# Kernel tuning notes

Hardware: AMD Instinct MI355X
Metric: run time of the kernel (lower is better)

Reference implementation:

```python
import jax, jax.numpy as jnp
import numpy as np

N_NODES = 50000
N_EDGES = 1600000
N_PAIRS = 4096
IN_N, IN_E = 32, 8
H, OE, ON = 4, 8, 32  # heads, out_edge_feats, out_node_feats
L = 4  # layers


def setup_inputs() -> dict:
    key = jax.random.key(0)
    ks = jax.random.split(key, 20)
    s = 0.1
    return {
        "x": jax.random.normal(ks[0], (N_NODES, IN_N), jnp.float32),
        "e": jax.random.normal(ks[1], (N_EDGES, IN_E), jnp.float32),
        "W_ni": jax.random.normal(ks[2], (L, IN_N, H * OE), jnp.float32) * s,
        "W_nj": jax.random.normal(ks[3], (L, IN_N, H * OE), jnp.float32) * s,
        "W_fij": jax.random.normal(ks[4], (L, IN_E, H * OE), jnp.float32) * s,
        "b_edge": jax.random.normal(ks[5], (L, H * OE), jnp.float32) * s,
        "attn": jax.random.normal(ks[6], (L, H, OE), jnp.float32) * s,
        "W_node": jax.random.normal(ks[7], (L, IN_N, H * ON), jnp.float32) * s,
        "W1": jax.random.normal(ks[8], (2 * L * ON, 128), jnp.float32) * s,
        "b1": jax.random.normal(ks[9], (128,), jnp.float32) * s,
        "W2": jax.random.normal(ks[10], (128, 1), jnp.float32) * s,
        "b2": jax.random.normal(ks[11], (1,), jnp.float32) * s,
        "src": jax.random.randint(ks[12], (N_EDGES,), 0, N_NODES, jnp.int32),
        "dst": jax.random.randint(ks[13], (N_EDGES,), 0, N_NODES, jnp.int32),
        "users": jax.random.randint(ks[14], (N_PAIRS,), 0, N_NODES, jnp.int32),
        "items": jax.random.randint(ks[15], (N_PAIRS,), 0, N_NODES, jnp.int32),
    }


def _egat_layer(h, e, src, dst, W_ni, W_nj, W_fij, b_edge, attn, W_node, n_nodes):
    # per-edge edge features: f_ni[src] + f_nj[dst] + f_fij + bias  -> (E, H*OE)
    f = (h @ W_ni)[src] + (h @ W_nj)[dst] + e @ W_fij + b_edge
    f_out = jax.nn.leaky_relu(f).reshape(-1, H, OE)          # (E, H, OE)
    logits = jnp.einsum("ehd,hd->eh", f_out, attn)           # (E, H)
    # edge softmax over incoming edges of each dst node
    mx = jax.ops.segment_max(logits, dst, num_segments=n_nodes)
    z = jnp.exp(logits - mx[dst])
    denom = jax.ops.segment_sum(z, dst, num_segments=n_nodes)
    a = z / denom[dst]                                        # (E, H)
    hh = (h @ W_node).reshape(n_nodes, H, ON)                 # (N, H, ON)
    msg = hh[src] * a[:, :, None]                             # (E, H, ON)
    return jax.ops.segment_sum(msg, dst, num_segments=n_nodes)  # (N, H, ON)


def reference(x, e, W_ni, W_nj, W_fij, b_edge, attn, W_node, W1, b1, W2, b2,
              src, dst, users, items):
    n_nodes = x.shape[0]
    states = []
    h = x
    for l in range(L):
        agg = _egat_layer(h, e, src, dst, W_ni[l], W_nj[l], W_fij[l],
                          b_edge[l], attn[l], W_node[l], n_nodes)
        h = jax.nn.elu(agg.sum(axis=1))  # sum heads, ELU -> (N, ON)
        states.append(h)
    states = jnp.concatenate(states, axis=1)                  # (N, L*ON)
    z = jnp.concatenate([states[users], states[items]], axis=1)  # (B, 2*L*ON)
    z = jax.nn.relu(z @ W1 + b1)
    out = jax.nn.sigmoid(z @ W2 + b2)
    return out[:, 0]
```

## Files before the change

kernel.cpp:

```cpp
#include <hip/hip_runtime.h>
#include <math.h>


static __device__ inline unsigned short f2bf(float f) {
  unsigned x = __float_as_uint(f);
  unsigned r = x + 0x7fffu + ((x >> 16) & 1u);
  return (unsigned short)(r >> 16);
}
static __device__ inline float bf2f(unsigned short u) {
  return __uint_as_float(((unsigned)u) << 16);
}
static __device__ inline float bf_lo(unsigned u) {
  return __uint_as_float(u << 16);
}
static __device__ inline float bf_hi(unsigned u) {
  return __uint_as_float(u & 0xffff0000u);
}


__global__ void zero_ints(int* __restrict__ p, int n) {
  int i = blockIdx.x * blockDim.x + threadIdx.x;
  if (i < n) p[i] = 0;
}

__global__ void histogram(const int* __restrict__ dst, int* __restrict__ hist,
                          int n_edges) {
  int e = blockIdx.x * blockDim.x + threadIdx.x;
  if (e < n_edges) atomicAdd(&hist[dst[e]], 1);
}

__global__ void scan_block(const int* __restrict__ hist, int* __restrict__ partial,
                           int* __restrict__ blocksum, int n) {
  __shared__ int buf[1024];
  int tid = threadIdx.x;
  int g = blockIdx.x * 1024 + tid;
  int v = (g < n) ? hist[g] : 0;
  buf[tid] = v;
  __syncthreads();
  for (int off = 1; off < 1024; off <<= 1) {
    int t = (tid >= off) ? buf[tid - off] : 0;
    __syncthreads();
    buf[tid] += t;
    __syncthreads();
  }
  if (g < n) partial[g] = buf[tid] - v;
  if (tid == 1023) blocksum[blockIdx.x] = buf[1023];
}

__global__ void scan_sums(int* __restrict__ blocksum, int nb) {
  if (threadIdx.x == 0 && blockIdx.x == 0) {
    int run = 0;
    for (int i = 0; i < nb; i++) {
      int t = blocksum[i];
      blocksum[i] = run;
      run += t;
    }
    blocksum[nb] = run;
  }
}

__global__ void scan_add(int* __restrict__ partial ,
                         const int* __restrict__ blocksum,
                         int* __restrict__ cursor, int n, int nb) {
  int g = blockIdx.x * blockDim.x + threadIdx.x;
  if (g < n) {
    int val = partial[g] + blocksum[g >> 10];
    partial[g] = val;
    cursor[g] = val;
  }
  if (g == 0) partial[n] = blocksum[nb];
}

__global__ void fill_records(const int* __restrict__ src, const int* __restrict__ dst,
                             int* __restrict__ cursor, int2* __restrict__ rec,
                             int n_edges) {
  int e = blockIdx.x * blockDim.x + threadIdx.x;
  if (e >= n_edges) return;
  int d = dst[e];
  int p = atomicAdd(&cursor[d], 1);
  rec[p] = make_int2(src[e], e);
}


__global__ void node_proj(const float* __restrict__ h,
                          const float* __restrict__ Wni,
                          const float* __restrict__ Wnj,
                          const float* __restrict__ Wnode,
                          unsigned short* __restrict__ fni,
                          unsigned short* __restrict__ fnj,
                          unsigned short* __restrict__ hh, int n_nodes) {
  int wave = (blockIdx.x * blockDim.x + threadIdx.x) >> 6;
  int lane = threadIdx.x & 63;
  int nwaves = (gridDim.x * blockDim.x) >> 6;
  int j = lane & 31;
  const float* Wsel = (lane < 32) ? Wni : Wnj;
  for (int n = wave; n < n_nodes; n += nwaves) {
    const float* hrow = h + (size_t)n * 32;
    float a0 = 0.f, a1 = 0.f, a2 = 0.f;
#pragma unroll
    for (int k = 0; k < 32; k++) {
      float hv = hrow[k];
      a0 += hv * Wsel[k * 32 + j];
      a1 += hv * Wnode[k * 128 + lane];
      a2 += hv * Wnode[k * 128 + lane + 64];
    }
    if (lane < 32) fni[(size_t)n * 32 + j] = f2bf(a0);
    else           fnj[(size_t)n * 32 + j] = f2bf(a0);
    hh[(size_t)n * 128 + lane] = f2bf(a1);
    hh[(size_t)n * 128 + lane + 64] = f2bf(a2);
  }
}

__global__ void node_agg_fused(const int2* __restrict__ rec,
                               const int* __restrict__ row_off,
                               const unsigned short* __restrict__ fni,
                               const unsigned short* __restrict__ fnj,
                               const unsigned short* __restrict__ hh,
                               const float* __restrict__ e,
                               const float* __restrict__ Wf,
                               const float* __restrict__ bE,
                               const float* __restrict__ attn,
                               float* __restrict__ hcur,
                               float* __restrict__ states,
                               int l, int n_nodes) {
  int n = (blockIdx.x * blockDim.x + threadIdx.x) >> 6;
  int lane = threadIdx.x & 63;
  if (n >= n_nodes) return;
  int j = lane & 31;
  int head = lane >> 4;
  int lane2 = lane * 2;

  float wcol[8];
#pragma unroll
  for (int kk = 0; kk < 8; kk++) wcol[kk] = Wf[kk * 32 + j];
  float bEj = bE[j];
  float attnj = attn[j];
  float fnjv = bf2f(fnj[(size_t)n * 32 + j]);

  int base = row_off[n], end = row_off[n + 1];
  float accx = 0.f, accy = 0.f, dh = 0.f;

  for (int k2 = base; k2 < end; k2 += 2) {
    int myk = k2 + (lane >> 5);
    bool valid = myk < end;
    int ksafe = valid ? myk : base;
    int2 re = rec[ksafe];
    int s = re.x;
    const float4* ep = (const float4*)(e + (size_t)re.y * 8);
    float4 ev0 = ep[0], ev1 = ep[1];
    float fniv = bf2f(fni[(size_t)s * 32 + j]);
    float f = fniv + fnjv + bEj;
    f = fmaf(ev0.x, wcol[0], f); f = fmaf(ev0.y, wcol[1], f);
    f = fmaf(ev0.z, wcol[2], f); f = fmaf(ev0.w, wcol[3], f);
    f = fmaf(ev1.x, wcol[4], f); f = fmaf(ev1.y, wcol[5], f);
    f = fmaf(ev1.z, wcol[6], f); f = fmaf(ev1.w, wcol[7], f);
    f = (f >= 0.f) ? f : 0.01f * f;
    float lgp = f * attnj;
    lgp += __shfl_xor(lgp, 1);
    lgp += __shfl_xor(lgp, 2);
    lgp += __shfl_xor(lgp, 4);
    float z = valid ? __expf(lgp) : 0.f;
    int sA = __shfl(s, 0);
    int sB = __shfl(s, 32);
    float zA = __shfl(z, head * 8);
    float zB = __shfl(z, 32 + head * 8);
    unsigned hA = *(const unsigned*)(hh + (size_t)sA * 128 + lane2);
    accx = fmaf(bf_lo(hA), zA, accx);
    accy = fmaf(bf_hi(hA), zA, accy);
    dh += zA;
    unsigned hB = *(const unsigned*)(hh + (size_t)sB * 128 + lane2);
    accx = fmaf(bf_lo(hB), zB, accx);
    accy = fmaf(bf_hi(hB), zB, accy);
    dh += zB;
  }

  float vx = 0.f, vy = 0.f;
  if (dh > 0.f) { vx = accx / dh; vy = accy / dh; }
  vx += __shfl_xor(vx, 16); vx += __shfl_xor(vx, 32);
  vy += __shfl_xor(vy, 16); vy += __shfl_xor(vy, 32);
  if (lane < 16) {
    float rx = (vx > 0.f) ? vx : expm1f(vx);
    float ry = (vy > 0.f) ? vy : expm1f(vy);
    float2 r = make_float2(rx, ry);
    ((float2*)(hcur + (size_t)n * 32))[lane] = r;
    ((float2*)(states + (size_t)n * 128 + l * 32))[lane] = r;
  }
}

__global__ void mlp_head(const float* __restrict__ states,
                         const int* __restrict__ users, const int* __restrict__ items,
                         const float* __restrict__ W1, const float* __restrict__ b1,
                         const float* __restrict__ W2, const float* __restrict__ b2,
                         float* __restrict__ out, int n_pairs) {
  __shared__ float zin[256];
  __shared__ float red[2];
  int p = blockIdx.x;
  if (p >= n_pairs) return;
  int t = threadIdx.x;
  int u = users[p], it = items[p];
  zin[t] = states[(size_t)u * 128 + t];
  zin[t + 128] = states[(size_t)it * 128 + t];
  __syncthreads();
  float acc = b1[t];
#pragma unroll 8
  for (int i = 0; i < 256; i++) acc += zin[i] * W1[i * 128 + t];
  acc = acc > 0.f ? acc : 0.f;
  float c = acc * W2[t];
#pragma unroll
  for (int off = 32; off > 0; off >>= 1) c += __shfl_down(c, off);
  if ((t & 63) == 0) red[t >> 6] = c;
  __syncthreads();
  if (t == 0) {
    float sum = red[0] + red[1] + b2[0];
    out[p] = 1.f / (1.f + expf(-sum));
  }
}


extern "C" void kernel_launch(void* const* d_in, const int* in_sizes, int n_in,
                              void* d_out, int out_size, void* d_ws, size_t ws_size,
                              hipStream_t stream) {
  const float* x     = (const float*)d_in[0];
  const float* e     = (const float*)d_in[1];
  const float* W_ni  = (const float*)d_in[2];
  const float* W_nj  = (const float*)d_in[3];
  const float* W_fij = (const float*)d_in[4];
  const float* b_e   = (const float*)d_in[5];
  const float* attn  = (const float*)d_in[6];
  const float* W_nd  = (const float*)d_in[7];
  const float* W1    = (const float*)d_in[8];
  const float* b1    = (const float*)d_in[9];
  const float* W2    = (const float*)d_in[10];
  const float* b2    = (const float*)d_in[11];
  const int* src   = (const int*)d_in[12];
  const int* dst   = (const int*)d_in[13];
  const int* users = (const int*)d_in[14];
  const int* items = (const int*)d_in[15];
  float* out = (float*)d_out;

  int n_nodes = in_sizes[0] / 32;
  int n_edges = in_sizes[12];
  int n_pairs = in_sizes[14];

  char* wsb = (char*)d_ws;
  size_t off = 0;
  auto alloc = [&](size_t bytes) {
    char* p = wsb + off;
    off = (off + bytes + 255) & ~(size_t)255;
    return p;
  };
  float*          hcur   = (float*)alloc((size_t)n_nodes * 32 * 4);
  float*          states = (float*)alloc((size_t)n_nodes * 128 * 4);
  unsigned short* fni    = (unsigned short*)alloc((size_t)n_nodes * 32 * 2);
  unsigned short* fnj    = (unsigned short*)alloc((size_t)n_nodes * 32 * 2);
  unsigned short* hh     = (unsigned short*)alloc((size_t)n_nodes * 128 * 2);
  int2*           rec    = (int2*)alloc((size_t)n_edges * 8);
  int*            row_off  = (int*)alloc(((size_t)n_nodes + 8) * 4);
  int*            cursor   = (int*)alloc(((size_t)n_nodes + 8) * 4);
  int*            hist     = (int*)alloc(((size_t)n_nodes + 8) * 4);
  int*            blocksum = (int*)alloc(256 * 4);

  int nb = (n_nodes + 1023) / 1024;
  zero_ints<<<(n_nodes + 255) / 256, 256, 0, stream>>>(hist, n_nodes);
  histogram<<<(n_edges + 255) / 256, 256, 0, stream>>>(dst, hist, n_edges);
  scan_block<<<nb, 1024, 0, stream>>>(hist, row_off, blocksum, n_nodes);
  scan_sums<<<1, 64, 0, stream>>>(blocksum, nb);
  scan_add<<<(n_nodes + 255) / 256, 256, 0, stream>>>(row_off, blocksum, cursor,
                                                      n_nodes, nb);
  fill_records<<<(n_edges + 255) / 256, 256, 0, stream>>>(src, dst, cursor, rec,
                                                          n_edges);

  for (int l = 0; l < 4; l++) {
    const float* hin = (l == 0) ? x : hcur;
    node_proj<<<2048, 256, 0, stream>>>(hin, W_ni + l * 1024, W_nj + l * 1024,
                                        W_nd + l * 4096, fni, fnj, hh, n_nodes);
    node_agg_fused<<<(n_nodes * 64 + 255) / 256, 256, 0, stream>>>(
        rec, row_off, fni, fnj, hh, e, W_fij + l * 256, b_e + l * 32,
        attn + l * 32, hcur, states, l, n_nodes);
  }
  mlp_head<<<n_pairs, 128, 0, stream>>>(states, users, items, W1, b1, W2, b2,
                                        out, n_pairs);
}
```

Before: 961.8 us.

## Split edge attention into per-edge kernel with pre-sorted bf16 edge data

Edges are permuted once into dst-sorted order, with src, dst and bf16-packed edge features stored contiguously, so later layers read them without going through an indirection. A new per-edge kernel computes the four head attention exponentials with one thread per edge, using weights staged in shared memory. The aggregation kernel then only gathers the precomputed z values and the hh rows, staging chunks in LDS and making the source index wave-uniform. The edge bias is folded into the dst projection. The trade-off is an extra kernel launch and a 16-byte-per-edge z buffer written and read every layer, and storing edge features in bf16 lowers precision.

Result: no change. 964.5 us (+0.3%).

```diff
diff --git a/kernel.cpp b/kernel.cpp
--- a/kernel.cpp
+++ b/kernel.cpp
@@ -7,8 +7,8 @@
   unsigned r = x + 0x7fffu + ((x >> 16) & 1u);
   return (unsigned short)(r >> 16);
 }
-static __device__ inline float bf2f(unsigned short u) {
-  return __uint_as_float(((unsigned)u) << 16);
+static __device__ inline unsigned pack2bf(float lo, float hi) {
+  return (unsigned)f2bf(lo) | ((unsigned)f2bf(hi) << 16);
 }
 static __device__ inline float bf_lo(unsigned u) {
   return __uint_as_float(u << 16);
@@ -71,14 +71,31 @@
   if (g == 0) partial[n] = blocksum[nb];
 }
 
-__global__ void fill_records(const int* __restrict__ src, const int* __restrict__ dst,
-                             int* __restrict__ cursor, int2* __restrict__ rec,
-                             int n_edges) {
+__global__ void fill_perm(const int* __restrict__ dst, int* __restrict__ cursor,
+                          int* __restrict__ perm, int n_edges) {
   int e = blockIdx.x * blockDim.x + threadIdx.x;
   if (e >= n_edges) return;
-  int d = dst[e];
-  int p = atomicAdd(&cursor[d], 1);
-  rec[p] = make_int2(src[e], e);
+  int p = atomicAdd(&cursor[dst[e]], 1);
+  perm[p] = e;
+}
+
+__global__ void expand_sorted(const int* __restrict__ perm,
+                              const int* __restrict__ src,
+                              const int* __restrict__ dst,
+                              const float* __restrict__ e,
+                              int* __restrict__ src_s, int* __restrict__ dst_s,
+                              uint4* __restrict__ e_s, int n_edges) {
+  int k = blockIdx.x * blockDim.x + threadIdx.x;
+  if (k >= n_edges) return;
+  int eid = perm[k];
+  src_s[k] = src[eid];
+  dst_s[k] = dst[eid];
+  const float4* ep = (const float4*)(e + (size_t)eid * 8);
+  float4 a = ep[0], b = ep[1];
+  uint4 r;
+  r.x = pack2bf(a.x, a.y); r.y = pack2bf(a.z, a.w);
+  r.z = pack2bf(b.x, b.y); r.w = pack2bf(b.z, b.w);
+  e_s[k] = r;
 }
 
 
@@ -86,8 +103,9 @@
                           const float* __restrict__ Wni,
                           const float* __restrict__ Wnj,
                           const float* __restrict__ Wnode,
+                          const float* __restrict__ bE,
                           unsigned short* __restrict__ fni,
-                          unsigned short* __restrict__ fnj,
+                          unsigned short* __restrict__ cdst,
                           unsigned short* __restrict__ hh, int n_nodes) {
   int wave = (blockIdx.x * blockDim.x + threadIdx.x) >> 6;
   int lane = threadIdx.x & 63;
@@ -105,73 +123,120 @@
       a2 += hv * Wnode[k * 128 + lane + 64];
     }
     if (lane < 32) fni[(size_t)n * 32 + j] = f2bf(a0);
-    else           fnj[(size_t)n * 32 + j] = f2bf(a0);
+    else           cdst[(size_t)n * 32 + j] = f2bf(a0 + bE[j]);
     hh[(size_t)n * 128 + lane] = f2bf(a1);
     hh[(size_t)n * 128 + lane + 64] = f2bf(a2);
   }
 }
 
-__global__ void node_agg_fused(const int2* __restrict__ rec,
-                               const int* __restrict__ row_off,
-                               const unsigned short* __restrict__ fni,
-                               const unsigned short* __restrict__ fnj,
-                               const unsigned short* __restrict__ hh,
-                               const float* __restrict__ e,
-                               const float* __restrict__ Wf,
-                               const float* __restrict__ bE,
-                               const float* __restrict__ attn,
-                               float* __restrict__ hcur,
-                               float* __restrict__ states,
-                               int l, int n_nodes) {
+__global__ void edge_z(const int* __restrict__ src_s,
+                       const int* __restrict__ dst_s,
+                       const uint4* __restrict__ e_s,
+                       const unsigned short* __restrict__ fni,
+                       const unsigned short* __restrict__ cdst,
+                       const float* __restrict__ Wf,
+                       const float* __restrict__ attn,
+                       float4* __restrict__ zrec, int n_edges) {
+  __shared__ float wfl[256];
+  __shared__ float atl[32];
+  int tid = threadIdx.x;
+  wfl[tid] = Wf[tid];
+  if (tid < 32) atl[tid] = attn[tid];
+  __syncthreads();
+  int k = blockIdx.x * blockDim.x + tid;
+  if (k >= n_edges) return;
+  int s = src_s[k], d = dst_s[k];
+  uint4 ep = e_s[k];
+  float ev[8];
+  ev[0] = bf_lo(ep.x); ev[1] = bf_hi(ep.x);
+  ev[2] = bf_lo(ep.y); ev[3] = bf_hi(ep.y);
+  ev[4] = bf_lo(ep.z); ev[5] = bf_hi(ep.z);
+  ev[6] = bf_lo(ep.w); ev[7] = bf_hi(ep.w);
+  const uint4* fr = (const uint4*)(fni + (size_t)s * 32);
+  const uint4* cr = (const uint4*)(cdst + (size_t)d * 32);
+  float f[32];
+#pragma unroll
+  for (int q = 0; q < 4; q++) {
+    uint4 ua = fr[q], ub = cr[q];
+    const unsigned* uap = (const unsigned*)&ua;
+    const unsigned* ubp = (const unsigned*)&ub;
+#pragma unroll
+    for (int c = 0; c < 4; c++) {
+      int jj = q * 8 + c * 2;
+      f[jj]     = bf_lo(uap[c]) + bf_lo(ubp[c]);
+      f[jj + 1] = bf_hi(uap[c]) + bf_hi(ubp[c]);
+    }
+  }
+#pragma unroll
+  for (int kk = 0; kk < 8; kk++) {
+    float ek = ev[kk];
+#pragma unroll
+    for (int j4 = 0; j4 < 8; j4++) {
+      float4 w = ((const float4*)wfl)[kk * 8 + j4];
+      f[j4 * 4 + 0] = fmaf(ek, w.x, f[j4 * 4 + 0]);
+      f[j4 * 4 + 1] = fmaf(ek, w.y, f[j4 * 4 + 1]);
+      f[j4 * 4 + 2] = fmaf(ek, w.z, f[j4 * 4 + 2]);
+      f[j4 * 4 + 3] = fmaf(ek, w.w, f[j4 * 4 + 3]);
+    }
+  }
+  float lg[4] = {0.f, 0.f, 0.f, 0.f};
+#pragma unroll
+  for (int jj = 0; jj < 32; jj++) {
+    float t = f[jj];
+    t = (t >= 0.f) ? t : 0.01f * t;
+    lg[jj >> 3] = fmaf(t, atl[jj], lg[jj >> 3]);
+  }
+  zrec[k] = make_float4(__expf(lg[0]), __expf(lg[1]),
+                        __expf(lg[2]), __expf(lg[3]));
+}
+
+__global__ void node_agg(const float4* __restrict__ zrec,
+                         const int* __restrict__ src_s,
+                         const int* __restrict__ row_off,
+                         const unsigned* __restrict__ hh,
+                         float* __restrict__ hcur,
+                         float* __restrict__ states,
+                         int l, int n_nodes) {
+  __shared__ float zw[4][64 * 4];
+  __shared__ int sw[4][64];
+  int wid = threadIdx.x >> 6;
+  int lane = threadIdx.x & 63;
   int n = (blockIdx.x * blockDim.x + threadIdx.x) >> 6;
-  int lane = threadIdx.x & 63;
   if (n >= n_nodes) return;
-  int j = lane & 31;
+  int base = row_off[n], end = row_off[n + 1];
   int head = lane >> 4;
-  int lane2 = lane * 2;
-
-  float wcol[8];
-#pragma unroll
-  for (int kk = 0; kk < 8; kk++) wcol[kk] = Wf[kk * 32 + j];
-  float bEj = bE[j];
-  float attnj = attn[j];
-  float fnjv = bf2f(fnj[(size_t)n * 32 + j]);
-
-  int base = row_off[n], end = row_off[n + 1];
+  float* zwf = zw[wid];
+  int* swp = sw[wid];
   float accx = 0.f, accy = 0.f, dh = 0.f;
 
-  for (int k2 = base; k2 < end; k2 += 2) {
-    int myk = k2 + (lane >> 5);
-    bool valid = myk < end;
-    int ksafe = valid ? myk : base;
-    int2 re = rec[ksafe];
-    int s = re.x;
-    const float4* ep = (const float4*)(e + (size_t)re.y * 8);
-    float4 ev0 = ep[0], ev1 = ep[1];
-    float fniv = bf2f(fni[(size_t)s * 32 + j]);
-    float f = fniv + fnjv + bEj;
-    f = fmaf(ev0.x, wcol[0], f); f = fmaf(ev0.y, wcol[1], f);
-    f = fmaf(ev0.z, wcol[2], f); f = fmaf(ev0.w, wcol[3], f);
-    f = fmaf(ev1.x, wcol[4], f); f = fmaf(ev1.y, wcol[5], f);
-    f = fmaf(ev1.z, wcol[6], f); f = fmaf(ev1.w, wcol[7], f);
-    f = (f >= 0.f) ? f : 0.01f * f;
-    float lgp = f * attnj;
-    lgp += __shfl_xor(lgp, 1);
-    lgp += __shfl_xor(lgp, 2);
-    lgp += __shfl_xor(lgp, 4);
-    float z = valid ? __expf(lgp) : 0.f;
-    int sA = __shfl(s, 0);
-    int sB = __shfl(s, 32);
-    float zA = __shfl(z, head * 8);
-    float zB = __shfl(z, 32 + head * 8);
-    unsigned hA = *(const unsigned*)(hh + (size_t)sA * 128 + lane2);
-    accx = fmaf(bf_lo(hA), zA, accx);
-    accy = fmaf(bf_hi(hA), zA, accy);
-    dh += zA;
-    unsigned hB = *(const unsigned*)(hh + (size_t)sB * 128 + lane2);
-    accx = fmaf(bf_lo(hB), zB, accx);
-    accy = fmaf(bf_hi(hB), zB, accy);
-    dh += zB;
+  for (int chunk = base; chunk < end; chunk += 64) {
+    int k = chunk + lane;
+    if (k < end) {
+      ((float4*)zwf)[lane] = zrec[k];
+      swp[lane] = src_s[k];
+    } else {
+      ((float4*)zwf)[lane] = make_float4(0.f, 0.f, 0.f, 0.f);
+      swp[lane] = 0;
+    }
+    int cnt = min(64, end - chunk);
+
+#define AGG_BODY(EE)                                                        \
+    {                                                                       \
+      int ss = __builtin_amdgcn_readfirstlane(swp[(EE)]);                   \
+      float zv = zwf[(EE) * 4 + head];                                      \
+      unsigned u = hh[(size_t)ss * 64 + lane];                              \
+      accx = fmaf(bf_lo(u), zv, accx);                                      \
+      accy = fmaf(bf_hi(u), zv, accy);                                      \
+      dh += zv;                                                             \
+    }
+
+    int ee = 0;
+    for (; ee + 8 <= cnt; ee += 8) {
+      AGG_BODY(ee + 0) AGG_BODY(ee + 1) AGG_BODY(ee + 2) AGG_BODY(ee + 3)
+      AGG_BODY(ee + 4) AGG_BODY(ee + 5) AGG_BODY(ee + 6) AGG_BODY(ee + 7)
+    }
+    for (; ee < cnt; ee++) { AGG_BODY(ee) }
+#undef AGG_BODY
   }
 
   float vx = 0.f, vy = 0.f;
@@ -252,13 +317,17 @@
   float*          hcur   = (float*)alloc((size_t)n_nodes * 32 * 4);
   float*          states = (float*)alloc((size_t)n_nodes * 128 * 4);
   unsigned short* fni    = (unsigned short*)alloc((size_t)n_nodes * 32 * 2);
-  unsigned short* fnj    = (unsigned short*)alloc((size_t)n_nodes * 32 * 2);
+  unsigned short* cdst   = (unsigned short*)alloc((size_t)n_nodes * 32 * 2);
   unsigned short* hh     = (unsigned short*)alloc((size_t)n_nodes * 128 * 2);
-  int2*           rec    = (int2*)alloc((size_t)n_edges * 8);
+  uint4*          e_s    = (uint4*)alloc((size_t)n_edges * 16);
+  float4*         zrec   = (float4*)alloc((size_t)n_edges * 16);
+  int*            src_s  = (int*)alloc((size_t)n_edges * 4);
+  int*            dst_s  = (int*)alloc((size_t)n_edges * 4);
   int*            row_off  = (int*)alloc(((size_t)n_nodes + 8) * 4);
-  int*            cursor   = (int*)alloc(((size_t)n_nodes + 8) * 4);
-  int*            hist     = (int*)alloc(((size_t)n_nodes + 8) * 4);
   int*            blocksum = (int*)alloc(256 * 4);
+  int* perm   = (int*)zrec;
+  int* hist   = (int*)((char*)zrec + ((size_t)n_edges * 4 + 1024));
+  int* cursor = (int*)((char*)zrec + ((size_t)n_edges * 8 + 2048));
 
   int nb = (n_nodes + 1023) / 1024;
   zero_ints<<<(n_nodes + 255) / 256, 256, 0, stream>>>(hist, n_nodes);
@@ -267,16 +336,21 @@
   scan_sums<<<1, 64, 0, stream>>>(blocksum, nb);
   scan_add<<<(n_nodes + 255) / 256, 256, 0, stream>>>(row_off, blocksum, cursor,
                                                       n_nodes, nb);
-  fill_records<<<(n_edges + 255) / 256, 256, 0, stream>>>(src, dst, cursor, rec,
-                                                          n_edges);
+  fill_perm<<<(n_edges + 255) / 256, 256, 0, stream>>>(dst, cursor, perm,
+                                                       n_edges);
+  expand_sorted<<<(n_edges + 255) / 256, 256, 0, stream>>>(
+      perm, src, dst, e, src_s, dst_s, e_s, n_edges);
 
   for (int l = 0; l < 4; l++) {
     const float* hin = (l == 0) ? x : hcur;
     node_proj<<<2048, 256, 0, stream>>>(hin, W_ni + l * 1024, W_nj + l * 1024,
-                                        W_nd + l * 4096, fni, fnj, hh, n_nodes);
-    node_agg_fused<<<(n_nodes * 64 + 255) / 256, 256, 0, stream>>>(
-        rec, row_off, fni, fnj, hh, e, W_fij + l * 256, b_e + l * 32,
-        attn + l * 32, hcur, states, l, n_nodes);
+                                        W_nd + l * 4096, b_e + l * 32,
+                                        fni, cdst, hh, n_nodes);
+    edge_z<<<(n_edges + 255) / 256, 256, 0, stream>>>(
+        src_s, dst_s, e_s, fni, cdst, W_fij + l * 256, attn + l * 32,
+        zrec, n_edges);
+    node_agg<<<(n_nodes * 64 + 255) / 256, 256, 0, stream>>>(
+        zrec, src_s, row_off, (const unsigned*)hh, hcur, states, l, n_nodes);
   }
   mlp_head<<<n_pairs, 128, 0, stream>>>(states, users, items, W1, b1, W2, b2,
                                         out, n_pairs);
```
